# Kernel optimization log

Measured on AMD Instinct MI355X. Metric: run time of the kernel, lower is better.

Reference implementation:

```python
import jax, jax.numpy as jnp
import numpy as np

B, S, D = 4, 2048, 1024
H, HK = 16, 4          # num_heads, num_heads_kv
HD = D // H            # head_dim = 64
G = H // HK            # kv groups = 4


def setup_inputs() -> dict:
    key = jax.random.key(0)
    ks = jax.random.split(key, 7)
    s = 0.02
    return {
        "query": jax.random.normal(ks[0], (B, S, D), jnp.float32),
        "key":   jax.random.normal(ks[1], (B, S, D), jnp.float32),
        "value": jax.random.normal(ks[2], (B, S, D), jnp.float32),
        # weights stored (in, out); equivalent to torch Linear y = x @ W.T
        "Wq": jax.random.normal(ks[3], (D, H * HD), jnp.float32) * s,
        "Wk": jax.random.normal(ks[4], (D, HK * HD), jnp.float32) * s,
        "Wv": jax.random.normal(ks[5], (D, HK * HD), jnp.float32) * s,
        "Wo": jax.random.normal(ks[6], (H * HD, D), jnp.float32) * s,
    }


def reference(query, key, value, Wq, Wk, Wv, Wo):
    b, qlen, _ = query.shape
    kvlen = key.shape[1]
    # projections
    q = (query @ Wq).reshape(b, qlen, H, HD)        # [b,q,H,hd]
    k = (key @ Wk).reshape(b, kvlen, HK, HD)        # [b,s,HK,hd]
    v = (value @ Wv).reshape(b, kvlen, HK, HD)      # [b,s,HK,hd]
    # GQA: q head h attends kv head h//G (repeat_interleave semantics)
    qg = q.reshape(b, qlen, HK, G, HD)              # head = kv*G + group
    scale = 1.0 / jnp.sqrt(jnp.asarray(HD, q.dtype))
    # scores [b,HK,G,q,s] -- broadcast kv heads, no materialized repeat
    scores = jnp.einsum('bqkgd,bskd->bkgqs', qg, k) * scale
    attn = jax.nn.softmax(scores, axis=-1)
    out = jnp.einsum('bkgqs,bskd->bqkgd', attn, v)  # [b,q,HK,G,hd]
    out = out.reshape(b, qlen, H * HD)
    return out @ Wo
```

## Files before the change

kernel.cpp:

```cpp
#include <hip/hip_runtime.h>


typedef unsigned short u16;
typedef unsigned int   u32;
typedef __bf16 bf16x4 __attribute__((ext_vector_type(4)));
typedef __bf16 bf16x8 __attribute__((ext_vector_type(8)));
typedef float  f32x4  __attribute__((ext_vector_type(4)));

#define MFMA(a,b,c) __builtin_amdgcn_mfma_f32_16x16x32_bf16((a),(b),(c),0,0,0)

#define GLDS(g, l) __builtin_amdgcn_global_load_lds(                          \
    (const __attribute__((address_space(1))) void*)(g),                       \
    (__attribute__((address_space(3))) void*)(l), 16, 0, 0)

#if __has_builtin(__builtin_amdgcn_exp2f)
#define EXP2(x) __builtin_amdgcn_exp2f(x)
#else
#define EXP2(x) exp2f(x)
#endif

__device__ __forceinline__ u16 f2bf(float f){
    u32 u = __builtin_bit_cast(u32, f);
    u += 0x7fffu + ((u >> 16) & 1u);
    return (u16)(u >> 16);
}
__device__ __forceinline__ u32 pk2(float a, float b){
#if __has_builtin(__builtin_amdgcn_cvt_pk_bf16_f32)
    auto r = __builtin_amdgcn_cvt_pk_bf16_f32(a, b);
    return __builtin_bit_cast(u32, r);
#else
    return (u32)f2bf(a) | ((u32)f2bf(b) << 16);
#endif
}
__device__ __forceinline__ bf16x8 ldfrag(const u16* p){
    return *(const bf16x8*)p;
}
__device__ __forceinline__ bf16x8 ld2x64(const u16* p){
    bf16x4 lo = *(const bf16x4*)p;
    bf16x4 hi = *(const bf16x4*)(p + 4);
    bf16x8 r;
    r[0]=lo[0]; r[1]=lo[1]; r[2]=lo[2]; r[3]=lo[3];
    r[4]=hi[0]; r[5]=hi[1]; r[6]=hi[2]; r[7]=hi[3];
    return r;
}

__global__ __launch_bounds__(256) void prep(const float* __restrict__ Wq,
                                            const float* __restrict__ Wk,
                                            const float* __restrict__ Wv,
                                            const float* __restrict__ Wo,
                                            u16* WqT, u16* WkT, u16* WvT, u16* WoT,
                                            const float* __restrict__ q,
                                            const float* __restrict__ k,
                                            const float* __restrict__ v,
                                            u16* Qa, u16* Ka, u16* Va){
    const int tid = threadIdx.x, bid = blockIdx.x;
    if (bid >= 2560){
        int j = bid - 2560;
        const float* src; u16* dst;
        if (j < 2048)      { src = q; dst = Qa; }
        else if (j < 4096) { src = k; dst = Ka; j -= 2048; }
        else               { src = v; dst = Va; j -= 4096; }
        size_t base = (size_t)j * 4096 + (size_t)tid * 16;
        float4 a = *(const float4*)(src + base);
        float4 b = *(const float4*)(src + base + 4);
        float4 c = *(const float4*)(src + base + 8);
        float4 d = *(const float4*)(src + base + 12);
        uint4 lo = make_uint4(pk2(a.x,a.y), pk2(a.z,a.w), pk2(b.x,b.y), pk2(b.z,b.w));
        uint4 hi = make_uint4(pk2(c.x,c.y), pk2(c.z,c.w), pk2(d.x,d.y), pk2(d.z,d.w));
        *(uint4*)(dst + base)     = lo;
        *(uint4*)(dst + base + 8) = hi;
        return;
    }
    __shared__ float T[32][33];
    const float* W; u16* WT; int N, i;
    if (bid < 1024)      { W = Wq; WT = WqT; N = 1024; i = bid; }
    else if (bid < 1280) { W = Wk; WT = WkT; N =  256; i = bid - 1024; }
    else if (bid < 1536) { W = Wv; WT = WvT; N =  256; i = bid - 1280; }
    else                 { W = Wo; WT = WoT; N = 1024; i = bid - 1536; }
    int kt = (i & 31) * 32, nt = (i >> 5) * 32;
    int r = tid >> 3, c = tid & 7;
    float4 vv = *(const float4*)(W + (size_t)(kt + r) * N + nt + c * 4);
    T[r][c*4+0] = vv.x; T[r][c*4+1] = vv.y; T[r][c*4+2] = vv.z; T[r][c*4+3] = vv.w;
    __syncthreads();
    u32 lo = pk2(T[c*4+0][r], T[c*4+1][r]);
    u32 hi = pk2(T[c*4+2][r], T[c*4+3][r]);
    *(uint2*)(WT + (size_t)(nt + r) * 1024 + kt + c * 4) = make_uint2(lo, hi);
}

template<int EPI>
__device__ __forceinline__ void gemm_body(const u16* __restrict__ A,
                                          const u16* __restrict__ Bt,
                                          void* __restrict__ Cp,
                                          int N, int K, int m0, int n0,
                                          u16* As, u16* Bs, float oscale){
    const int tid  = threadIdx.x;
    const int wave = tid >> 6, lane = tid & 63;
    const int quad = lane >> 4, l15 = lane & 15;
    const int wm = wave >> 1, wn = wave & 1;
    const int srow = lane >> 3;
    const int scol = ((lane & 7) ^ srow) * 8;
    const int swz  = l15 & 7;

    f32x4 acc[4][4];
    #pragma unroll
    for (int i = 0; i < 4; ++i)
        #pragma unroll
        for (int j = 0; j < 4; ++j) acc[i][j] = (f32x4){0.f, 0.f, 0.f, 0.f};

    const int nkt = K >> 6;
    for (int kt = 0; kt < nkt; ++kt){
        if (kt) __syncthreads();
        {
            const u16* ga = A + (size_t)(m0 + wave*32 + srow) * K + kt*64 + scol;
            #pragma unroll
            for (int p = 0; p < 4; ++p)
                GLDS(ga + (size_t)(p*8) * K, As + (wave*32 + p*8) * 64);
        }
        {
            const u16* gb = Bt + (size_t)(n0 + wave*32 + srow) * K + kt*64 + scol;
            #pragma unroll
            for (int p = 0; p < 4; ++p)
                GLDS(gb + (size_t)(p*8) * K, Bs + (wave*32 + p*8) * 64);
        }
        __syncthreads();
        #pragma unroll
        for (int ks = 0; ks < 2; ++ks){
            bf16x8 af[4], bfr[4];
            #pragma unroll
            for (int mt = 0; mt < 4; ++mt)
                af[mt] = ldfrag(&As[(wm*64 + mt*16 + l15) * 64 +
                                    (((ks*4 + quad) ^ swz) * 8)]);
            #pragma unroll
            for (int nt = 0; nt < 4; ++nt)
                bfr[nt] = ldfrag(&Bs[(wn*64 + nt*16 + l15) * 64 +
                                     (((ks*4 + quad) ^ swz) * 8)]);
            #pragma unroll
            for (int mt = 0; mt < 4; ++mt)
                #pragma unroll
                for (int nt = 0; nt < 4; ++nt){
                    if constexpr (EPI == 1)
                        acc[mt][nt] = MFMA(af[mt], bfr[nt], acc[mt][nt]);
                    else
                        acc[mt][nt] = MFMA(bfr[nt], af[mt], acc[mt][nt]);
                }
        }
    }
    #pragma unroll
    for (int mt = 0; mt < 4; ++mt){
        #pragma unroll
        for (int nt = 0; nt < 4; ++nt){
            if constexpr (EPI == 1){
                int rowb = m0 + wm*64 + mt*16 + quad*4;
                int col  = n0 + wn*64 + nt*16 + l15;
                u16* C = (u16*)Cp;
                int bb = rowb >> 11, s = rowb & 2047;
                u32 lo = pk2(acc[mt][nt][0], acc[mt][nt][1]);
                u32 hi = pk2(acc[mt][nt][2], acc[mt][nt][3]);
                *(uint2*)(C + (size_t)(bb * 256 + col) * 2048 + s) = make_uint2(lo, hi);
            } else {
                int row  = m0 + wm*64 + mt*16 + l15;
                int colb = n0 + wn*64 + nt*16 + quad*4;
                if constexpr (EPI == 0){
                    u16* C = (u16*)Cp;
                    u32 lo = pk2(acc[mt][nt][0]*oscale, acc[mt][nt][1]*oscale);
                    u32 hi = pk2(acc[mt][nt][2]*oscale, acc[mt][nt][3]*oscale);
                    *(uint2*)(C + (size_t)row * N + colb) = make_uint2(lo, hi);
                } else {
                    float* C = (float*)Cp;
                    *(f32x4*)(C + (size_t)row * N + colb) = acc[mt][nt];
                }
            }
        }
    }
}

__global__ __launch_bounds__(256) void gemm_qkv(const u16* Qa, const u16* WqT, u16* Qp,
                                                const u16* Ka, const u16* WkT, u16* Kp,
                                                const u16* Va, const u16* WvT, u16* Vt,
                                                float qscale){
    __shared__ u16 As[128 * 64];
    __shared__ u16 Bs[128 * 64];
    int bid = blockIdx.x;
    if (bid < 512){
        int x = bid & 7, s = bid >> 3;
        int m = x * 8 + (s >> 3), n = s & 7;
        gemm_body<0>(Qa, WqT, (void*)Qp, 1024, 1024,
                     m * 128, n * 128, As, Bs, qscale);
    } else if (bid < 640){
        int i = bid - 512;
        int x = i & 7, s = i >> 3;
        int m = x * 8 + (s >> 1), n = s & 1;
        gemm_body<0>(Ka, WkT, (void*)Kp, 256, 1024,
                     m * 128, n * 128, As, Bs, 1.0f);
    } else {
        int i = bid - 640;
        int x = i & 7, s = i >> 3;
        int m = x * 8 + (s >> 1), n = s & 1;
        gemm_body<1>(Va, WvT, (void*)Vt, 256, 1024,
                     m * 128, n * 128, As, Bs, 1.0f);
    }
}

__global__ __launch_bounds__(256) void gemm_o(const u16* AO, const u16* WoT,
                                              float* Out){
    __shared__ u16 As[128 * 64];
    __shared__ u16 Bs[128 * 64];
    int bid = blockIdx.x;
    int x = bid & 7, s = bid >> 3;
    int m = x * 8 + (s >> 3), n = s & 7;
    gemm_body<2>(AO, WoT, (void*)Out, 1024, 1024,
                 m * 128, n * 128, As, Bs, 1.0f);
}

__global__ __launch_bounds__(512, 4) void attn_k(const u16* __restrict__ Qp,
                                                 const u16* __restrict__ Kp,
                                                 const u16* __restrict__ Vt,
                                                 u16* __restrict__ AO){
    constexpr int S = 2048, Dm = 1024, NKV = 256, PST = 68;
    __shared__ u16 Kb[2][64 * 64];
    __shared__ u16 Vb[2][64 * 64];
    __shared__ u16 Ps[256 * PST];
    const int tid = threadIdx.x, wave = tid >> 6, lane = tid & 63;
    const int quad = lane >> 4, l15 = lane & 15;
    const int h = blockIdx.y, b = blockIdx.z;
    const int hk = h >> 2, q0 = blockIdx.x * 256;
    u16* pw = Ps + wave * (32 * PST);

    const int srow = lane >> 3;
    const int scol = ((lane & 7) ^ srow) * 8;
    const int swz  = l15 & 7;

    auto issue = [&](int t){
        int j0 = t * 64, bufi = t & 1;
        int r = wave * 8 + srow;
        GLDS(Kp + (size_t)(b * S + j0 + r) * NKV + hk * 64 + scol,
             &Kb[bufi][wave * 8 * 64]);
        GLDS(Vt + (size_t)(b * NKV + hk * 64 + r) * S + j0 + scol,
             &Vb[bufi][wave * 8 * 64]);
    };

    issue(0);
    {
        int c8 = tid & 7, r0 = tid >> 3;
        #pragma unroll
        for (int p = 0; p < 4; ++p){
            int r = r0 + p * 64;
            uint4 v = *(const uint4*)(Qp + (size_t)(b * S + q0 + r) * Dm + h * 64 + c8 * 8);
            *(uint2*)&Ps[r * PST + c8 * 8]     = make_uint2(v.x, v.y);
            *(uint2*)&Ps[r * PST + c8 * 8 + 4] = make_uint2(v.z, v.w);
        }
    }
    __syncthreads();
    bf16x8 qf[2][2];
    #pragma unroll
    for (int mt = 0; mt < 2; ++mt)
        #pragma unroll
        for (int ks = 0; ks < 2; ++ks)
            qf[mt][ks] = ld2x64(&Ps[(wave*32 + mt*16 + l15) * PST + ks*32 + quad*8]);

    const u32 one2 = 0x3F803F80u;
    const bf16x8 ones = __builtin_bit_cast(bf16x8, make_uint4(one2, one2, one2, one2));

    f32x4 O[4][2];
    #pragma unroll
    for (int dt = 0; dt < 4; ++dt)
        #pragma unroll
        for (int mt = 0; mt < 2; ++mt) O[dt][mt] = (f32x4){0.f, 0.f, 0.f, 0.f};
    f32x4 sums[2];
    #pragma unroll
    for (int mt = 0; mt < 2; ++mt) sums[mt] = (f32x4){0.f, 0.f, 0.f, 0.f};

    for (int t = 0; t < 32; ++t){
        __syncthreads();
        if (t < 31) issue(t + 1);
        const u16* Kt = Kb[t & 1];
        const u16* Vs = Vb[t & 1];
        f32x4 sf[2][4];
        #pragma unroll
        for (int mt = 0; mt < 2; ++mt)
            #pragma unroll
            for (int nt = 0; nt < 4; ++nt) sf[mt][nt] = (f32x4){0.f, 0.f, 0.f, 0.f};
        #pragma unroll
        for (int ks = 0; ks < 2; ++ks){
            bf16x8 ak[4];
            #pragma unroll
            for (int nt = 0; nt < 4; ++nt)
                ak[nt] = ldfrag(&Kt[(nt*16 + l15) * 64 + (((ks*4 + quad) ^ swz) * 8)]);
            #pragma unroll
            for (int mt = 0; mt < 2; ++mt)
                #pragma unroll
                for (int nt = 0; nt < 4; ++nt)
                    sf[mt][nt] = MFMA(ak[nt], qf[mt][ks], sf[mt][nt]);
        }
        #pragma unroll
        for (int mt = 0; mt < 2; ++mt)
            #pragma unroll
            for (int nt = 0; nt < 4; ++nt){
                float e0 = EXP2(sf[mt][nt][0]);
                float e1 = EXP2(sf[mt][nt][1]);
                float e2 = EXP2(sf[mt][nt][2]);
                float e3 = EXP2(sf[mt][nt][3]);
                *(uint2*)&pw[(mt*16 + l15) * PST + nt*16 + quad*4] =
                    make_uint2(pk2(e0, e1), pk2(e2, e3));
            }
        __threadfence_block();
        #pragma unroll
        for (int ks = 0; ks < 2; ++ks){
            bf16x8 av[4], bp[2];
            #pragma unroll
            for (int dt = 0; dt < 4; ++dt)
                av[dt] = ldfrag(&Vs[(dt*16 + l15) * 64 + (((ks*4 + quad) ^ swz) * 8)]);
            #pragma unroll
            for (int mt = 0; mt < 2; ++mt)
                bp[mt] = ld2x64(&pw[(mt*16 + l15) * PST + ks*32 + quad*8]);
            #pragma unroll
            for (int mt = 0; mt < 2; ++mt)
                sums[mt] = MFMA(ones, bp[mt], sums[mt]);
            #pragma unroll
            for (int dt = 0; dt < 4; ++dt)
                #pragma unroll
                for (int mt = 0; mt < 2; ++mt)
                    O[dt][mt] = MFMA(av[dt], bp[mt], O[dt][mt]);
        }
    }
    #pragma unroll
    for (int mt = 0; mt < 2; ++mt){
        float inv = 1.0f / sums[mt][0];
        size_t row = (size_t)(b * S + q0 + wave*32 + mt*16 + l15);
        #pragma unroll
        for (int dt = 0; dt < 4; ++dt){
            u32 lo = pk2(O[dt][mt][0] * inv, O[dt][mt][1] * inv);
            u32 hi = pk2(O[dt][mt][2] * inv, O[dt][mt][3] * inv);
            *(uint2*)(AO + row * Dm + h * 64 + dt*16 + quad*4) = make_uint2(lo, hi);
        }
    }
}

extern "C" void kernel_launch(void* const* d_in, const int* in_sizes, int n_in,
                              void* d_out, int out_size, void* d_ws, size_t ws_size,
                              hipStream_t stream){
    const float* q  = (const float*)d_in[0];
    const float* k  = (const float*)d_in[1];
    const float* v  = (const float*)d_in[2];
    const float* Wq = (const float*)d_in[3];
    const float* Wk = (const float*)d_in[4];
    const float* Wv = (const float*)d_in[5];
    const float* Wo = (const float*)d_in[6];
    char* ws = (char*)d_ws;
    const size_t MB = 1u << 20;
    u16* WqT = (u16*)(ws);
    u16* WkT = (u16*)(ws + 2*MB);
    u16* WvT = (u16*)(ws + 2*MB + 512*1024);
    u16* WoT = (u16*)(ws + 3*MB);
    u16* Qp  = (u16*)(ws + 5*MB);
    u16* Kp  = (u16*)(ws + 21*MB);
    u16* Vt  = (u16*)(ws + 25*MB);
    u16* AO  = (u16*)(ws + 29*MB);
    u16* Qa  = (u16*)(ws + 29*MB);
    u16* Ka  = (u16*)(ws + 45*MB);
    u16* Va  = (u16*)(ws + 61*MB);

    const float cexp = 0.125f * 1.44269504f;

    prep<<<dim3(8704), 256, 0, stream>>>(Wq, Wk, Wv, Wo, WqT, WkT, WvT, WoT,
                                         q, k, v, Qa, Ka, Va);
    gemm_qkv<<<dim3(768), 256, 0, stream>>>(Qa, WqT, Qp, Ka, WkT, Kp,
                                            Va, WvT, Vt, cexp);
    attn_k<<<dim3(8, 16, 4), 512, 0, stream>>>(Qp, Kp, Vt, AO);
    gemm_o<<<dim3(512), 256, 0, stream>>>(AO, WoT, (float*)d_out);
}
```

Baseline: 307.0 us.

## Enlarge GEMM tiles to 256x256 with 512 threads and double-buffered LDS

The QKV and output projection GEMMs move from 128x128 tiles with 256 threads to 256x256 tiles with 512 threads, and each wave now owns a 128x64 output slab. The K-loop is double-buffered: the next K-tile is loaded into LDS while the current one is consumed, which removes one barrier per iteration. The aim is more data reuse per loaded tile and overlap of loads with MFMA work. The cost is a much smaller grid (192 and 128 blocks), which may leave many of the GPU's CUs idle, plus higher LDS and register use per block.

```diff
diff --git a/kernel.cpp b/kernel.cpp
--- a/kernel.cpp
+++ b/kernel.cpp
@@ -93,49 +93,59 @@
                                           void* __restrict__ Cp,
                                           int N, int K, int m0, int n0,
                                           u16* As, u16* Bs, float oscale){
+    constexpr int TSZ = 256 * 64;
     const int tid  = threadIdx.x;
     const int wave = tid >> 6, lane = tid & 63;
     const int quad = lane >> 4, l15 = lane & 15;
-    const int wm = wave >> 1, wn = wave & 1;
+    const int wm = wave >> 2, wn = wave & 3;
     const int srow = lane >> 3;
     const int scol = ((lane & 7) ^ srow) * 8;
     const int swz  = l15 & 7;
 
-    f32x4 acc[4][4];
-    #pragma unroll
-    for (int i = 0; i < 4; ++i)
+    f32x4 acc[8][4];
+    #pragma unroll
+    for (int i = 0; i < 8; ++i)
         #pragma unroll
         for (int j = 0; j < 4; ++j) acc[i][j] = (f32x4){0.f, 0.f, 0.f, 0.f};
 
     const int nkt = K >> 6;
-    for (int kt = 0; kt < nkt; ++kt){
-        if (kt) __syncthreads();
-        {
-            const u16* ga = A + (size_t)(m0 + wave*32 + srow) * K + kt*64 + scol;
-            #pragma unroll
-            for (int p = 0; p < 4; ++p)
-                GLDS(ga + (size_t)(p*8) * K, As + (wave*32 + p*8) * 64);
-        }
-        {
-            const u16* gb = Bt + (size_t)(n0 + wave*32 + srow) * K + kt*64 + scol;
-            #pragma unroll
-            for (int p = 0; p < 4; ++p)
-                GLDS(gb + (size_t)(p*8) * K, Bs + (wave*32 + p*8) * 64);
-        }
-        __syncthreads();
+    auto issueA = [&](int kt, u16* la){
+        const u16* ga = A + (size_t)(m0 + wave*32 + srow) * K + kt*64 + scol;
+        #pragma unroll
+        for (int p = 0; p < 4; ++p)
+            GLDS(ga + (size_t)(p*8) * K, la + (wave*32 + p*8) * 64);
+    };
+    auto issueB = [&](int kt, u16* lb){
+        const u16* gb = Bt + (size_t)(n0 + wave*32 + srow) * K + kt*64 + scol;
+        #pragma unroll
+        for (int p = 0; p < 4; ++p)
+            GLDS(gb + (size_t)(p*8) * K, lb + (wave*32 + p*8) * 64);
+    };
+
+    issueA(0, As);
+    issueB(0, Bs);
+    __syncthreads();
+
+    for (int t = 0; t < nkt; ++t){
+        const u16* Asc = As + (t & 1) * TSZ;
+        const u16* Bsc = Bs + (t & 1) * TSZ;
+        if (t + 1 < nkt){
+            issueA(t + 1, As + ((t & 1) ^ 1) * TSZ);
+            issueB(t + 1, Bs + ((t & 1) ^ 1) * TSZ);
+        }
         #pragma unroll
         for (int ks = 0; ks < 2; ++ks){
-            bf16x8 af[4], bfr[4];
-            #pragma unroll
-            for (int mt = 0; mt < 4; ++mt)
-                af[mt] = ldfrag(&As[(wm*64 + mt*16 + l15) * 64 +
-                                    (((ks*4 + quad) ^ swz) * 8)]);
+            bf16x8 af[8], bfr[4];
+            #pragma unroll
+            for (int mt = 0; mt < 8; ++mt)
+                af[mt] = ldfrag(&Asc[(wm*128 + mt*16 + l15) * 64 +
+                                     (((ks*4 + quad) ^ swz) * 8)]);
             #pragma unroll
             for (int nt = 0; nt < 4; ++nt)
-                bfr[nt] = ldfrag(&Bs[(wn*64 + nt*16 + l15) * 64 +
-                                     (((ks*4 + quad) ^ swz) * 8)]);
-            #pragma unroll
-            for (int mt = 0; mt < 4; ++mt)
+                bfr[nt] = ldfrag(&Bsc[(wn*64 + nt*16 + l15) * 64 +
+                                      (((ks*4 + quad) ^ swz) * 8)]);
+            #pragma unroll
+            for (int mt = 0; mt < 8; ++mt)
                 #pragma unroll
                 for (int nt = 0; nt < 4; ++nt){
                     if constexpr (EPI == 1)
@@ -144,13 +154,15 @@
                         acc[mt][nt] = MFMA(bfr[nt], af[mt], acc[mt][nt]);
                 }
         }
-    }
-    #pragma unroll
-    for (int mt = 0; mt < 4; ++mt){
+        __syncthreads();
+    }
+
+    #pragma unroll
+    for (int mt = 0; mt < 8; ++mt){
         #pragma unroll
         for (int nt = 0; nt < 4; ++nt){
             if constexpr (EPI == 1){
-                int rowb = m0 + wm*64 + mt*16 + quad*4;
+                int rowb = m0 + wm*128 + mt*16 + quad*4;
                 int col  = n0 + wn*64 + nt*16 + l15;
                 u16* C = (u16*)Cp;
                 int bb = rowb >> 11, s = rowb & 2047;
@@ -158,7 +170,7 @@
                 u32 hi = pk2(acc[mt][nt][2], acc[mt][nt][3]);
                 *(uint2*)(C + (size_t)(bb * 256 + col) * 2048 + s) = make_uint2(lo, hi);
             } else {
-                int row  = m0 + wm*64 + mt*16 + l15;
+                int row  = m0 + wm*128 + mt*16 + l15;
                 int colb = n0 + wn*64 + nt*16 + quad*4;
                 if constexpr (EPI == 0){
                     u16* C = (u16*)Cp;
@@ -174,42 +186,42 @@
     }
 }
 
-__global__ __launch_bounds__(256) void gemm_qkv(const u16* Qa, const u16* WqT, u16* Qp,
+__global__ __launch_bounds__(512) void gemm_qkv(const u16* Qa, const u16* WqT, u16* Qp,
                                                 const u16* Ka, const u16* WkT, u16* Kp,
                                                 const u16* Va, const u16* WvT, u16* Vt,
                                                 float qscale){
-    __shared__ u16 As[128 * 64];
-    __shared__ u16 Bs[128 * 64];
+    __shared__ u16 As[2 * 256 * 64];
+    __shared__ u16 Bs[2 * 256 * 64];
     int bid = blockIdx.x;
-    if (bid < 512){
+    if (bid < 128){
         int x = bid & 7, s = bid >> 3;
-        int m = x * 8 + (s >> 3), n = s & 7;
+        int m = x * 4 + (s >> 2), n = s & 3;
         gemm_body<0>(Qa, WqT, (void*)Qp, 1024, 1024,
-                     m * 128, n * 128, As, Bs, qscale);
-    } else if (bid < 640){
-        int i = bid - 512;
+                     m * 256, n * 256, As, Bs, qscale);
+    } else if (bid < 160){
+        int i = bid - 128;
         int x = i & 7, s = i >> 3;
-        int m = x * 8 + (s >> 1), n = s & 1;
+        int m = x * 4 + s;
         gemm_body<0>(Ka, WkT, (void*)Kp, 256, 1024,
-                     m * 128, n * 128, As, Bs, 1.0f);
+                     m * 256, 0, As, Bs, 1.0f);
     } else {
-        int i = bid - 640;
+        int i = bid - 160;
         int x = i & 7, s = i >> 3;
-        int m = x * 8 + (s >> 1), n = s & 1;
+        int m = x * 4 + s;
         gemm_body<1>(Va, WvT, (void*)Vt, 256, 1024,
-                     m * 128, n * 128, As, Bs, 1.0f);
-    }
-}
-
-__global__ __launch_bounds__(256) void gemm_o(const u16* AO, const u16* WoT,
+                     m * 256, 0, As, Bs, 1.0f);
+    }
+}
+
+__global__ __launch_bounds__(512) void gemm_o(const u16* AO, const u16* WoT,
                                               float* Out){
-    __shared__ u16 As[128 * 64];
-    __shared__ u16 Bs[128 * 64];
+    __shared__ u16 As[2 * 256 * 64];
+    __shared__ u16 Bs[2 * 256 * 64];
     int bid = blockIdx.x;
     int x = bid & 7, s = bid >> 3;
-    int m = x * 8 + (s >> 3), n = s & 7;
+    int m = x * 4 + (s >> 2), n = s & 3;
     gemm_body<2>(AO, WoT, (void*)Out, 1024, 1024,
-                 m * 128, n * 128, As, Bs, 1.0f);
+                 m * 256, n * 256, As, Bs, 1.0f);
 }
 
 __global__ __launch_bounds__(512, 4) void attn_k(const u16* __restrict__ Qp,
@@ -364,8 +376,8 @@
 
     prep<<<dim3(8704), 256, 0, stream>>>(Wq, Wk, Wv, Wo, WqT, WkT, WvT, WoT,
                                          q, k, v, Qa, Ka, Va);
-    gemm_qkv<<<dim3(768), 256, 0, stream>>>(Qa, WqT, Qp, Ka, WkT, Kp,
+    gemm_qkv<<<dim3(192), 512, 0, stream>>>(Qa, WqT, Qp, Ka, WkT, Kp,
                                             Va, WvT, Vt, cexp);
     attn_k<<<dim3(8, 16, 4), 512, 0, stream>>>(Qp, Kp, Vt, AO);
-    gemm_o<<<dim3(512), 256, 0, stream>>>(AO, WoT, (float*)d_out);
-}
+    gemm_o<<<dim3(128), 512, 0, stream>>>(AO, WoT, (float*)d_out);
+}
```

Result: no change. 312.8 us (+1.9%).
